# Performance work log

Hardware: AMD Instinct MI355X
Metric: run time of the kernel (lower is better)

The kernel has to match this reference:

```python
import jax, jax.numpy as jnp
import numpy as np


def setup_inputs() -> dict:
    key = jax.random.key(0)
    k1, k2, k3 = jax.random.split(key, 3)
    C, H, W = 64, 1024, 1024          # feature map from the UNet embed model
    N_PIX = H * W                      # every pixel belongs to one superpixel
    N_SEG = 4096                       # number of superpixels
    features = jax.random.normal(k1, (C, H, W), dtype=jnp.float32)
    pix_yx = jax.random.randint(k2, (N_PIX, 2), 0, H)          # (y, x) coords per pixel entry
    segment_ids = jax.random.randint(k3, (N_PIX,), 0, N_SEG)   # superpixel id per pixel entry
    return {"features": features, "pix_yx": pix_yx,
            "segment_ids": segment_ids, "n_segments": N_SEG}


def reference(features, pix_yx, segment_ids, n_segments):
    # features: [C, H, W]; pix_yx: [N, 2]; segment_ids: [N]
    # Equivalent to: for each superpixel i, mean of features[:, sp[:,-2], sp[:,-1]] over its pixels.
    gathered = features[:, pix_yx[:, 0], pix_yx[:, 1]].T          # [N, C] irregular gather
    sums = jax.ops.segment_sum(gathered, segment_ids,
                               num_segments=n_segments)           # [S, C]
    counts = jax.ops.segment_sum(jnp.ones_like(segment_ids, dtype=features.dtype),
                                 segment_ids, num_segments=n_segments)  # [S]
    # original asserts mass > 0; guard divide for any empty segment
    return sums / jnp.maximum(counts, 1.0)[:, None]               # [S, C]
```

## Files before the change

### kernel.cpp

```cpp
#include <hip/hip_runtime.h>
#include <stdint.h>

#define CCH 64
#define HW  (1024 * 1024)
#define NPIX (1024 * 1024)
#define NSEG 4096
#define NBIN 65536

#define WS_NEED ((size_t)147456 * 1024)

__device__ inline uint32_t pack_bf16(float a, float b) {
    uint32_t ua = __float_as_uint(a), ub = __float_as_uint(b);
    ua = (ua + 0x7FFFu + ((ua >> 16) & 1u)) >> 16;
    ub = (ub + 0x7FFFu + ((ub >> 16) & 1u)) >> 16;
    return (ub << 16) | ua;
}
__device__ inline float bf_lo(uint32_t v) { return __uint_as_float(v << 16); }
__device__ inline float bf_hi(uint32_t v) { return __uint_as_float(v & 0xFFFF0000u); }

__global__ void k1_pack_hist(const int* __restrict__ pix_yx,
                             const int* __restrict__ seg,
                             uint32_t* __restrict__ packed,
                             uint32_t* __restrict__ poshist,
                             uint32_t* __restrict__ seghistPad) {
    int n = blockIdx.x * blockDim.x + threadIdx.x;
    int2 yx = ((const int2*)pix_yx)[n];
    uint32_t s = (uint32_t)seg[n];
    uint32_t pos = ((uint32_t)yx.x << 10) | (uint32_t)yx.y;
    packed[n] = (s << 20) | pos;
    atomicAdd(&poshist[pos >> 4], 1u);
    atomicAdd(&seghistPad[s * 16], 1u);
}

__global__ void k2a_scan_local(const uint32_t* __restrict__ poshist,
                               uint32_t* __restrict__ posLocal,
                               uint32_t* __restrict__ posBlk) {
    __shared__ uint32_t sh[1024];
    int t = threadIdx.x, b = blockIdx.x;
    int i = b * 1024 + t;
    uint32_t v = poshist[i];
    sh[t] = v;
    __syncthreads();
    for (int off = 1; off < 1024; off <<= 1) {
        uint32_t u = (t >= off) ? sh[t - off] : 0u;
        __syncthreads();
        sh[t] += u;
        __syncthreads();
    }
    uint32_t inc = sh[t];
    posLocal[i] = inc - v;
    if (t == 1023) posBlk[b] = inc;
}

__global__ void k2b_scan_tops(const uint32_t* __restrict__ posBlk,
                              uint32_t* __restrict__ posBlkExc,
                              const uint32_t* __restrict__ seghistPad,
                              uint32_t* __restrict__ segOff,
                              uint32_t* __restrict__ segCursorPad) {
    int t = threadIdx.x;
    if (t < 64) {
        uint32_t v = posBlk[t];
        uint32_t x = v;
        for (int off = 1; off < 64; off <<= 1) {
            uint32_t u = __shfl_up(x, off);
            if ((t & 63) >= off) x += u;
        }
        posBlkExc[t] = x - v;
    }
    uint32_t c0 = seghistPad[(4 * t + 0) * 16];
    uint32_t c1 = seghistPad[(4 * t + 1) * 16];
    uint32_t c2 = seghistPad[(4 * t + 2) * 16];
    uint32_t c3 = seghistPad[(4 * t + 3) * 16];
    uint32_t tot = c0 + c1 + c2 + c3;
    __shared__ uint32_t sh[1024];
    sh[t] = tot;
    __syncthreads();
    for (int off = 1; off < 1024; off <<= 1) {
        uint32_t u = (t >= off) ? sh[t - off] : 0u;
        __syncthreads();
        sh[t] += u;
        __syncthreads();
    }
    uint32_t base = sh[t] - tot;
    uint32_t o0 = base, o1 = base + c0, o2 = o1 + c1, o3 = o2 + c2;
    ((uint4*)segOff)[t] = make_uint4(o0, o1, o2, o3);
    segCursorPad[(4 * t + 0) * 16] = o0;
    segCursorPad[(4 * t + 1) * 16] = o1;
    segCursorPad[(4 * t + 2) * 16] = o2;
    segCursorPad[(4 * t + 3) * 16] = o3;
}

__global__ void k2c_scan_add(const uint32_t* __restrict__ posLocal,
                             const uint32_t* __restrict__ posBlkExc,
                             uint32_t* __restrict__ posCursorPad) {
    int t = threadIdx.x, b = blockIdx.x;
    int i = b * 1024 + t;
    posCursorPad[(size_t)i * 16] = posLocal[i] + posBlkExc[b];
}

__global__ void k3_scatter(const uint32_t* __restrict__ packed,
                           uint32_t* __restrict__ posCursorPad,
                           uint32_t* __restrict__ sorted) {
    int n = blockIdx.x * blockDim.x + threadIdx.x;
    uint32_t p = packed[n];
    uint32_t d = atomicAdd(&posCursorPad[(size_t)((p & 0xFFFFFu) >> 4) * 16], 1u);
    sorted[d] = p;
}

__global__ __launch_bounds__(256) void k4_gather(const float* __restrict__ feat,
                                                 const uint32_t* __restrict__ sorted,
                                                 uint32_t* __restrict__ segCursorPad,
                                                 uint32_t* __restrict__ gathered) {
    __shared__ uint32_t epack[1024];
    __shared__ uint32_t rnk[1024];
    __shared__ uint32_t tile_pk[64 * 33];
    const int tid = threadIdx.x;
    const int w = tid >> 6;
    const int l = tid & 63;
    const int base = blockIdx.x * 1024;

#pragma unroll
    for (int i = 0; i < 4; ++i) epack[tid + 256 * i] = sorted[base + tid + 256 * i];
    __syncthreads();
#pragma unroll
    for (int i = 0; i < 4; ++i) {
        int idx = tid * 4 + i;
        uint32_t sg = epack[idx] >> 20;
        rnk[idx] = atomicAdd(&segCursorPad[sg * 16], 1u);
    }
    __syncthreads();

    for (int t = 0; t < 16; ++t) {
        uint32_t pk = epack[t * 64 + l];
        const float* fp = feat + (pk & 0xFFFFFu);
#pragma unroll
        for (int kk = 0; kk < 8; ++kk) {
            int k = w * 8 + kk;
            float a = fp[(size_t)(2 * k) * HW];
            float b = fp[(size_t)(2 * k + 1) * HW];
            tile_pk[l * 33 + k] = pack_bf16(a, b);
        }
        __syncthreads();
#pragma unroll
        for (int pp = 0; pp < 16; pp += 2) {
            int p = w * 16 + pp + (l >> 5);
            int k = l & 31;
            uint32_t r = rnk[t * 64 + p];
            gathered[(size_t)r * 32 + k] = tile_pk[p * 33 + k];
        }
        __syncthreads();
    }
}

__global__ __launch_bounds__(256) void k5_reduce(const uint32_t* __restrict__ gathered,
                                                 const uint32_t* __restrict__ segOff,
                                                 const uint32_t* __restrict__ seghistPad,
                                                 float* __restrict__ out) {
    const int s = blockIdx.x;
    const int tid = threadIdx.x;
    const int k = tid & 31;
    const int sub = tid >> 5;
    uint32_t base = segOff[s];
    uint32_t cnt = seghistPad[s * 16];
    float a0 = 0.f, a1 = 0.f;
    for (uint32_t r = sub; r < cnt; r += 8) {
        uint32_t v = gathered[(size_t)(base + r) * 32 + k];
        a0 += bf_lo(v);
        a1 += bf_hi(v);
    }
    __shared__ float red0[8][32];
    __shared__ float red1[8][32];
    red0[sub][k] = a0;
    red1[sub][k] = a1;
    __syncthreads();
    if (tid < 32) {
        float s0 = 0.f, s1 = 0.f;
#pragma unroll
        for (int j = 0; j < 8; ++j) { s0 += red0[j][tid]; s1 += red1[j][tid]; }
        float inv = 1.0f / (float)(cnt ? cnt : 1u);
        ((float2*)out)[s * 32 + tid] = make_float2(s0 * inv, s1 * inv);
    }
}

__global__ __launch_bounds__(256) void k4_stream(const float* __restrict__ feat,
                                                 const uint32_t* __restrict__ sorted,
                                                 float* __restrict__ sums) {
    __shared__ float tile[64 * 65];
    __shared__ uint32_t epack[1024];
    const int tid = threadIdx.x;
    const int w = tid >> 6;
    const int l = tid & 63;
    const int base = blockIdx.x * 1024;
    for (int i = tid; i < 1024; i += 256) epack[i] = sorted[base + i];
    __syncthreads();
    for (int t = 0; t < 16; ++t) {
        uint32_t pk = epack[t * 64 + l];
        const float* fp = feat + (pk & 0xFFFFFu);
#pragma unroll
        for (int cc = 0; cc < 16; ++cc) {
            int c = (w << 4) + cc;
            tile[l * 65 + c] = fp[(size_t)c * HW];
        }
        __syncthreads();
#pragma unroll
        for (int pp = 0; pp < 16; ++pp) {
            int p = (w << 4) + pp;
            uint32_t sg = epack[t * 64 + p] >> 20;
            atomicAdd(&sums[sg * 64 + l], tile[p * 65 + l]);
        }
        __syncthreads();
    }
}

__global__ void k5_div(float* __restrict__ out, const uint32_t* __restrict__ seghistPad) {
    int i = blockIdx.x * blockDim.x + threadIdx.x;
    uint32_t cnt = seghistPad[(i >> 6) * 16];
    float c = (float)(cnt ? cnt : 1u);
    out[i] = out[i] / c;
}

extern "C" void kernel_launch(void* const* d_in, const int* in_sizes, int n_in,
                              void* d_out, int out_size, void* d_ws, size_t ws_size,
                              hipStream_t stream) {
    const float* feat = (const float*)d_in[0];
    const int*   pix  = (const int*)d_in[1];
    const int*   seg  = (const int*)d_in[2];
    float* out = (float*)d_out;

    uint8_t* ws = (uint8_t*)d_ws;
    uint32_t* packed       = (uint32_t*)(ws);
    uint32_t* sortedPos    = (uint32_t*)(ws + (size_t)4096 * 1024);
    uint32_t* poshist      = (uint32_t*)(ws + (size_t)8192 * 1024);
    uint32_t* posLocal     = (uint32_t*)(ws + (size_t)8448 * 1024);
    uint32_t* posBlk       = (uint32_t*)(ws + (size_t)8704 * 1024);
    uint32_t* posBlkExc    = (uint32_t*)(ws + (size_t)8708 * 1024);
    uint32_t* segOff       = (uint32_t*)(ws + (size_t)8712 * 1024);
    uint32_t* seghistPad   = (uint32_t*)(ws + (size_t)8736 * 1024);
    uint32_t* segCursorPad = (uint32_t*)(ws + (size_t)8992 * 1024);
    uint32_t* posCursorPad = (uint32_t*)(ws + (size_t)10240 * 1024);
    uint32_t* gathered     = (uint32_t*)(ws + (size_t)16384 * 1024);

    hipMemsetAsync(poshist, 0, (size_t)NBIN * sizeof(uint32_t), stream);
    hipMemsetAsync(seghistPad, 0, (size_t)NSEG * 16 * sizeof(uint32_t), stream);
    hipMemsetAsync(out, 0, (size_t)NSEG * CCH * sizeof(float), stream);

    k1_pack_hist<<<NPIX / 256, 256, 0, stream>>>(pix, seg, packed, poshist, seghistPad);
    k2a_scan_local<<<64, 1024, 0, stream>>>(poshist, posLocal, posBlk);
    k2b_scan_tops<<<1, 1024, 0, stream>>>(posBlk, posBlkExc, seghistPad, segOff, segCursorPad);
    k2c_scan_add<<<64, 1024, 0, stream>>>(posLocal, posBlkExc, posCursorPad);
    k3_scatter<<<NPIX / 256, 256, 0, stream>>>(packed, posCursorPad, sortedPos);

    if (ws_size >= WS_NEED) {
        k4_gather<<<NPIX / 1024, 256, 0, stream>>>(feat, sortedPos, segCursorPad, gathered);
        k5_reduce<<<NSEG, 256, 0, stream>>>(gathered, segOff, seghistPad, out);
    } else {
        k4_stream<<<NPIX / 1024, 256, 0, stream>>>(feat, sortedPos, out);
        k5_div<<<(NSEG * CCH) / 256, 256, 0, stream>>>(out, seghistPad);
    }
}
```

Baseline: 650.2 us.

## Simplify gather to per-thread row writes with nontemporal stores, vectorize pack/scatter

The gather kernel drops its shared-memory transpose tile and block syncs. Each thread now takes one sorted pixel, claims its rank atomically, reads all 64 channels, and writes a full 128-byte bf16 row as vector nontemporal stores. The reduce reads that buffer with nontemporal loads, and the pack/histogram and scatter kernels each handle two pixels per thread. The workspace layout is reordered so one memset clears both histograms. The per-thread channel loads are uncoalesced across lanes, unlike the old tile layout, which may cost more in load efficiency than is saved on syncs.

```diff
diff --git a/kernel.cpp b/kernel.cpp
--- a/kernel.cpp
+++ b/kernel.cpp
@@ -7,6 +7,8 @@
 #define NSEG 4096
 #define NBIN 65536
 
+typedef uint32_t u32x4 __attribute__((ext_vector_type(4)));
+
 #define WS_NEED ((size_t)147456 * 1024)
 
 __device__ inline uint32_t pack_bf16(float a, float b) {
@@ -18,18 +20,22 @@
 __device__ inline float bf_lo(uint32_t v) { return __uint_as_float(v << 16); }
 __device__ inline float bf_hi(uint32_t v) { return __uint_as_float(v & 0xFFFF0000u); }
 
-__global__ void k1_pack_hist(const int* __restrict__ pix_yx,
-                             const int* __restrict__ seg,
-                             uint32_t* __restrict__ packed,
+__global__ void k1_pack_hist(const int4* __restrict__ pix2,
+                             const int2* __restrict__ seg2,
+                             uint2* __restrict__ packed2,
                              uint32_t* __restrict__ poshist,
                              uint32_t* __restrict__ seghistPad) {
     int n = blockIdx.x * blockDim.x + threadIdx.x;
-    int2 yx = ((const int2*)pix_yx)[n];
-    uint32_t s = (uint32_t)seg[n];
-    uint32_t pos = ((uint32_t)yx.x << 10) | (uint32_t)yx.y;
-    packed[n] = (s << 20) | pos;
-    atomicAdd(&poshist[pos >> 4], 1u);
-    atomicAdd(&seghistPad[s * 16], 1u);
+    int4 yx = pix2[n];
+    int2 ss = seg2[n];
+    uint32_t pos0 = ((uint32_t)yx.x << 10) | (uint32_t)yx.y;
+    uint32_t pos1 = ((uint32_t)yx.z << 10) | (uint32_t)yx.w;
+    packed2[n] = make_uint2(((uint32_t)ss.x << 20) | pos0,
+                            ((uint32_t)ss.y << 20) | pos1);
+    atomicAdd(&poshist[pos0 >> 4], 1u);
+    atomicAdd(&poshist[pos1 >> 4], 1u);
+    atomicAdd(&seghistPad[(uint32_t)ss.x * 16], 1u);
+    atomicAdd(&seghistPad[(uint32_t)ss.y * 16], 1u);
 }
 
 __global__ void k2a_scan_local(const uint32_t* __restrict__ poshist,
@@ -98,57 +104,40 @@
     posCursorPad[(size_t)i * 16] = posLocal[i] + posBlkExc[b];
 }
 
-__global__ void k3_scatter(const uint32_t* __restrict__ packed,
+__global__ void k3_scatter(const uint2* __restrict__ packed2,
                            uint32_t* __restrict__ posCursorPad,
                            uint32_t* __restrict__ sorted) {
     int n = blockIdx.x * blockDim.x + threadIdx.x;
-    uint32_t p = packed[n];
-    uint32_t d = atomicAdd(&posCursorPad[(size_t)((p & 0xFFFFFu) >> 4) * 16], 1u);
-    sorted[d] = p;
+    uint2 p = packed2[n];
+    uint32_t d0 = atomicAdd(&posCursorPad[(size_t)((p.x & 0xFFFFFu) >> 4) * 16], 1u);
+    uint32_t d1 = atomicAdd(&posCursorPad[(size_t)((p.y & 0xFFFFFu) >> 4) * 16], 1u);
+    sorted[d0] = p.x;
+    sorted[d1] = p.y;
 }
 
 __global__ __launch_bounds__(256) void k4_gather(const float* __restrict__ feat,
                                                  const uint32_t* __restrict__ sorted,
                                                  uint32_t* __restrict__ segCursorPad,
                                                  uint32_t* __restrict__ gathered) {
-    __shared__ uint32_t epack[1024];
-    __shared__ uint32_t rnk[1024];
-    __shared__ uint32_t tile_pk[64 * 33];
-    const int tid = threadIdx.x;
-    const int w = tid >> 6;
-    const int l = tid & 63;
-    const int base = blockIdx.x * 1024;
-
-#pragma unroll
-    for (int i = 0; i < 4; ++i) epack[tid + 256 * i] = sorted[base + tid + 256 * i];
-    __syncthreads();
-#pragma unroll
-    for (int i = 0; i < 4; ++i) {
-        int idx = tid * 4 + i;
-        uint32_t sg = epack[idx] >> 20;
-        rnk[idx] = atomicAdd(&segCursorPad[sg * 16], 1u);
-    }
-    __syncthreads();
-
-    for (int t = 0; t < 16; ++t) {
-        uint32_t pk = epack[t * 64 + l];
-        const float* fp = feat + (pk & 0xFFFFFu);
-#pragma unroll
-        for (int kk = 0; kk < 8; ++kk) {
-            int k = w * 8 + kk;
-            float a = fp[(size_t)(2 * k) * HW];
-            float b = fp[(size_t)(2 * k + 1) * HW];
-            tile_pk[l * 33 + k] = pack_bf16(a, b);
-        }
-        __syncthreads();
-#pragma unroll
-        for (int pp = 0; pp < 16; pp += 2) {
-            int p = w * 16 + pp + (l >> 5);
-            int k = l & 31;
-            uint32_t r = rnk[t * 64 + p];
-            gathered[(size_t)r * 32 + k] = tile_pk[p * 33 + k];
-        }
-        __syncthreads();
+    int idx = blockIdx.x * blockDim.x + threadIdx.x;
+    uint32_t pk = sorted[idx];
+    uint32_t sg = pk >> 20;
+    const float* fp = feat + (pk & 0xFFFFFu);
+    uint32_t r = atomicAdd(&segCursorPad[sg * 16], 1u);
+    u32x4* dst = (u32x4*)(gathered + (size_t)r * 32);
+#pragma unroll
+    for (int j = 0; j < 8; ++j) {
+        float a0 = fp[(size_t)(8 * j + 0) * HW];
+        float b0 = fp[(size_t)(8 * j + 1) * HW];
+        float a1 = fp[(size_t)(8 * j + 2) * HW];
+        float b1 = fp[(size_t)(8 * j + 3) * HW];
+        float a2 = fp[(size_t)(8 * j + 4) * HW];
+        float b2 = fp[(size_t)(8 * j + 5) * HW];
+        float a3 = fp[(size_t)(8 * j + 6) * HW];
+        float b3 = fp[(size_t)(8 * j + 7) * HW];
+        u32x4 v = { pack_bf16(a0, b0), pack_bf16(a1, b1),
+                    pack_bf16(a2, b2), pack_bf16(a3, b3) };
+        __builtin_nontemporal_store(v, dst + j);
     }
 }
 
@@ -164,7 +153,7 @@
     uint32_t cnt = seghistPad[s * 16];
     float a0 = 0.f, a1 = 0.f;
     for (uint32_t r = sub; r < cnt; r += 8) {
-        uint32_t v = gathered[(size_t)(base + r) * 32 + k];
+        uint32_t v = __builtin_nontemporal_load(&gathered[(size_t)(base + r) * 32 + k]);
         a0 += bf_lo(v);
         a1 += bf_hi(v);
     }
@@ -231,27 +220,27 @@
     uint32_t* packed       = (uint32_t*)(ws);
     uint32_t* sortedPos    = (uint32_t*)(ws + (size_t)4096 * 1024);
     uint32_t* poshist      = (uint32_t*)(ws + (size_t)8192 * 1024);
-    uint32_t* posLocal     = (uint32_t*)(ws + (size_t)8448 * 1024);
-    uint32_t* posBlk       = (uint32_t*)(ws + (size_t)8704 * 1024);
-    uint32_t* posBlkExc    = (uint32_t*)(ws + (size_t)8708 * 1024);
-    uint32_t* segOff       = (uint32_t*)(ws + (size_t)8712 * 1024);
-    uint32_t* seghistPad   = (uint32_t*)(ws + (size_t)8736 * 1024);
-    uint32_t* segCursorPad = (uint32_t*)(ws + (size_t)8992 * 1024);
+    uint32_t* seghistPad   = (uint32_t*)(ws + (size_t)8448 * 1024);
+    uint32_t* posLocal     = (uint32_t*)(ws + (size_t)8704 * 1024);
+    uint32_t* posBlk       = (uint32_t*)(ws + (size_t)8960 * 1024);
+    uint32_t* posBlkExc    = (uint32_t*)(ws + (size_t)8964 * 1024);
+    uint32_t* segOff       = (uint32_t*)(ws + (size_t)8968 * 1024);
+    uint32_t* segCursorPad = (uint32_t*)(ws + (size_t)9216 * 1024);
     uint32_t* posCursorPad = (uint32_t*)(ws + (size_t)10240 * 1024);
     uint32_t* gathered     = (uint32_t*)(ws + (size_t)16384 * 1024);
 
-    hipMemsetAsync(poshist, 0, (size_t)NBIN * sizeof(uint32_t), stream);
-    hipMemsetAsync(seghistPad, 0, (size_t)NSEG * 16 * sizeof(uint32_t), stream);
+    hipMemsetAsync(poshist, 0, (size_t)512 * 1024, stream);
     hipMemsetAsync(out, 0, (size_t)NSEG * CCH * sizeof(float), stream);
 
-    k1_pack_hist<<<NPIX / 256, 256, 0, stream>>>(pix, seg, packed, poshist, seghistPad);
+    k1_pack_hist<<<NPIX / 512, 256, 0, stream>>>((const int4*)pix, (const int2*)seg,
+                                                 (uint2*)packed, poshist, seghistPad);
     k2a_scan_local<<<64, 1024, 0, stream>>>(poshist, posLocal, posBlk);
     k2b_scan_tops<<<1, 1024, 0, stream>>>(posBlk, posBlkExc, seghistPad, segOff, segCursorPad);
     k2c_scan_add<<<64, 1024, 0, stream>>>(posLocal, posBlkExc, posCursorPad);
-    k3_scatter<<<NPIX / 256, 256, 0, stream>>>(packed, posCursorPad, sortedPos);
+    k3_scatter<<<NPIX / 512, 256, 0, stream>>>((const uint2*)packed, posCursorPad, sortedPos);
 
     if (ws_size >= WS_NEED) {
-        k4_gather<<<NPIX / 1024, 256, 0, stream>>>(feat, sortedPos, segCursorPad, gathered);
+        k4_gather<<<NPIX / 256, 256, 0, stream>>>(feat, sortedPos, segCursorPad, gathered);
         k5_reduce<<<NSEG, 256, 0, stream>>>(gathered, segOff, seghistPad, out);
     } else {
         k4_stream<<<NPIX / 1024, 256, 0, stream>>>(feat, sortedPos, out);
```

Result: slower. 956.0 us (+47.0%).
